# Optimization experiments

Hardware: AMD Instinct MI355X
Metric: run time of the kernel (lower is better)

## Reference

```python
import jax, jax.numpy as jnp
import numpy as np

B, N, C_IN, C_OUT, K, D_EMB = 64, 2048, 64, 64, 3, 10

def setup_inputs() -> dict:
    key = jax.random.key(0)
    k1, k2, k3, k4 = jax.random.split(key, 4)
    x = jax.random.normal(k1, (B, N, C_IN), dtype=jnp.float32)
    node_embeddings = jax.random.normal(k2, (N, D_EMB), dtype=jnp.float32)
    weights_pool = jax.random.normal(k3, (D_EMB, K, C_IN, C_OUT), dtype=jnp.float32) * 0.1
    bias_pool = jax.random.normal(k4, (D_EMB, C_OUT), dtype=jnp.float32) * 0.1
    return {"x": x, "node_embeddings": node_embeddings,
            "weights_pool": weights_pool, "bias_pool": bias_pool, "cheb_k": K}

def reference(x, node_embeddings, weights_pool, bias_pool, cheb_k):
    n = node_embeddings.shape[0]
    # adaptive adjacency: softmax over rows of relu(E E^T)
    supports = jax.nn.softmax(jax.nn.relu(node_embeddings @ node_embeddings.T), axis=1)  # [N,N]
    support_set = [jnp.eye(n, dtype=x.dtype), supports]
    for _ in range(2, cheb_k):
        support_set.append(2.0 * supports @ support_set[-1] - support_set[-2])
    supports_k = jnp.stack(support_set, axis=0)                     # [K,N,N]
    # per-node weights/bias generated from embedding
    weights = jnp.einsum('nd,dkio->nkio', node_embeddings, weights_pool)  # [N,K,Ci,Co]
    bias = node_embeddings @ bias_pool                               # [N,Co]
    # graph conv: gather Chebyshev-filtered features then per-node grouped GEMM
    x_g = jnp.einsum('knm,bmc->bnkc', supports_k, x)                 # [B,N,K,Ci]
    out = jnp.einsum('bnki,nkio->bno', x_g, weights) + bias          # [B,N,Co]
    return out
```

## Files before the change

### kernel.cpp

```cpp
#include <hip/hip_runtime.h>

typedef __attribute__((ext_vector_type(8))) short short8;
typedef __attribute__((ext_vector_type(4))) float f32x4;
typedef __attribute__((ext_vector_type(4))) unsigned short us4;
typedef __attribute__((ext_vector_type(8))) unsigned short us8;

constexpr int Bb = 64, Nn = 2048, CI = 64, CO = 64, KK = 3, DE = 10;
constexpr int NW = Bb * CI;
constexpr int WPSZ = KK * CI * CO;

__device__ __forceinline__ unsigned short f2bf(float f) {
  unsigned u = __float_as_uint(f);
  u += 0x7fff + ((u >> 16) & 1);
  return (unsigned short)(u >> 16);
}
__device__ __forceinline__ float bf2f(unsigned short h) {
  return __uint_as_float(((unsigned)h) << 16);
}
__device__ __forceinline__ void gl2lds16(const void* g, void* l) {
  __builtin_amdgcn_global_load_lds(
      (const __attribute__((address_space(1))) void*)g,
      (__attribute__((address_space(3))) void*)l, 16, 0, 0);
}

__global__ __launch_bounds__(256) void prep_kernel(
    const float* __restrict__ E, unsigned short* __restrict__ S,
    const float* __restrict__ x, unsigned short* __restrict__ Xrow,
    unsigned short* __restrict__ XT, const float* __restrict__ Wp,
    unsigned short* __restrict__ Wpf) {
  __shared__ float sh[5376];
  const int bid = blockIdx.x, t = threadIdx.x;

  if (bid < 2048) {
    const int n = bid;
    float emb[DE];
#pragma unroll
    for (int d = 0; d < DE; d++) emb[d] = E[n * DE + d];

    float v[8];
    for (int h = 0; h < 4; h++) {
      __syncthreads();
      const float* src = E + (size_t)(512 * DE) * h;
#pragma unroll
      for (int q = 0; q < 5; q++) {
        const int idx = t + q * 256;
        *(float4*)&sh[idx * 4] = *(const float4*)(src + idx * 4);
      }
      __syncthreads();
#pragma unroll
      for (int jj = 0; jj < 2; jj++) {
        const int lm = t + jj * 256;
        const float2* er = (const float2*)&sh[lm * 10];
        float dot = 0.f;
#pragma unroll
        for (int p = 0; p < 5; p++) {
          const float2 e2 = er[p];
          dot += emb[2 * p] * e2.x + emb[2 * p + 1] * e2.y;
        }
        v[h * 2 + jj] = fmaxf(dot, 0.f);
      }
    }

    float* red = &sh[5120];
    float lmax = -1e30f;
#pragma unroll
    for (int j = 0; j < 8; j++) lmax = fmaxf(lmax, v[j]);
    red[t] = lmax;
    __syncthreads();
    for (int s = 128; s > 0; s >>= 1) {
      if (t < s) red[t] = fmaxf(red[t], red[t + s]);
      __syncthreads();
    }
    const float rowmax = red[0];
    __syncthreads();
    float lsum = 0.f;
#pragma unroll
    for (int j = 0; j < 8; j++) { v[j] = __expf(v[j] - rowmax); lsum += v[j]; }
    red[t] = lsum;
    __syncthreads();
    for (int s = 128; s > 0; s >>= 1) {
      if (t < s) red[t] += red[t + s];
      __syncthreads();
    }
    const float inv = 1.f / red[0];
#pragma unroll
    for (int j = 0; j < 8; j++) S[(size_t)n * Nn + t + j * 256] = f2bf(v[j] * inv);
  } else if (bid < 4096) {
    const int id = bid - 2048;
    const int b = id & 63, n0 = (id >> 6) * 64;
    const int i4 = (t & 15) * 4;
#pragma unroll
    for (int j = 0; j < 4; j++) {
      const int r = j * 16 + (t >> 4);
      const float4 v =
          *(const float4*)(x + (size_t)b * (Nn * CI) + (size_t)(n0 + r) * CI + i4);
      us4 o; o.x = f2bf(v.x); o.y = f2bf(v.y); o.z = f2bf(v.z); o.w = f2bf(v.w);
      *(us4*)(Xrow + (size_t)(n0 + r) * NW + b * CI + i4) = o;
      sh[r * 65 + i4 + 0] = v.x; sh[r * 65 + i4 + 1] = v.y;
      sh[r * 65 + i4 + 2] = v.z; sh[r * 65 + i4 + 3] = v.w;
    }
    __syncthreads();
    const int i = t >> 2, c0 = (t & 3) * 16;
    us8 p0, p1;
#pragma unroll
    for (int j = 0; j < 8; j++) p0[j] = f2bf(sh[(c0 + j) * 65 + i]);
#pragma unroll
    for (int j = 0; j < 8; j++) p1[j] = f2bf(sh[(c0 + 8 + j) * 65 + i]);
    unsigned short* dst = XT + (size_t)(b * CI + i) * Nn + n0 + c0;
    *(us8*)(dst) = p0;
    *(us8*)(dst + 8) = p1;
  } else {
    const int e4 = ((bid - 4096) * 256 + t) * 4;
    const int d = e4 / WPSZ;
    const int r = e4 - d * WPSZ;
    const int c = r >> 12, io = r & 4095;
    float4 v = *(const float4*)(Wp + (size_t)d * WPSZ + c * 4096 + io);
    if (c == 0) {
      const float4 w2 = *(const float4*)(Wp + (size_t)d * WPSZ + 2 * 4096 + io);
      v.x -= w2.x; v.y -= w2.y; v.z -= w2.z; v.w -= w2.w;
    } else if (c == 2) {
      v.x *= 2.f; v.y *= 2.f; v.z *= 2.f; v.w *= 2.f;
    }
    us4 o; o.x = f2bf(v.x); o.y = f2bf(v.y); o.z = f2bf(v.z); o.w = f2bf(v.w);
    *(us4*)(Wpf + e4) = o;
  }
}

__global__ __launch_bounds__(256) void mfma_gemm(
    const unsigned short* __restrict__ A, const unsigned short* __restrict__ Bt,
    unsigned short* __restrict__ Crow, unsigned short* __restrict__ Ct, int mode) {
  __shared__ unsigned short sm[12288];
  unsigned short* As = sm;
  unsigned short* Bs = sm + 8192;
  const int t = threadIdx.x, lane = t & 63, wave = t >> 6;
  const int n0 = blockIdx.x * 64, m0 = blockIdx.y * 128;
  const int wm = (wave & 1) * 64, wn = (wave >> 1) * 32;
  const int lr = lane & 15, lq = lane >> 4;

  f32x4 acc[4][2] = {};
  const int srow = lane >> 3;
  const int schunk = (lane & 7) ^ srow;

  for (int k0 = 0; k0 < 2048; k0 += 64) {
    __syncthreads();
#pragma unroll
    for (int j = 0; j < 4; j++) {
      const int r0 = (wave * 4 + j) * 8;
      gl2lds16(A + (size_t)(m0 + r0 + srow) * 2048 + k0 + schunk * 8, As + r0 * 64);
    }
#pragma unroll
    for (int j = 0; j < 2; j++) {
      const int r0 = (wave * 2 + j) * 8;
      gl2lds16(Bt + (size_t)(n0 + r0 + srow) * 2048 + k0 + schunk * 8, Bs + r0 * 64);
    }
    __syncthreads();
#pragma unroll
    for (int ks = 0; ks < 2; ks++) {
      short8 af[4], bfr[2];
#pragma unroll
      for (int i = 0; i < 4; i++) {
        const int m = wm + i * 16 + lr;
        const int slot = (ks * 4 + lq) ^ (m & 7);
        af[i] = *(const short8*)(As + m * 64 + slot * 8);
      }
#pragma unroll
      for (int j = 0; j < 2; j++) {
        const int n = wn + j * 16 + lr;
        const int slot = (ks * 4 + lq) ^ (n & 7);
        bfr[j] = *(const short8*)(Bs + n * 64 + slot * 8);
      }
#pragma unroll
      for (int i = 0; i < 4; i++)
#pragma unroll
        for (int j = 0; j < 2; j++)
          acc[i][j] = __builtin_amdgcn_mfma_f32_16x16x32_bf16(af[i], bfr[j], acc[i][j], 0, 0, 0);
    }
  }

  __syncthreads();
#pragma unroll
  for (int i = 0; i < 4; i++) {
#pragma unroll
    for (int r = 0; r < 4; r++) {
      const int m = wm + i * 16 + lq * 4 + r;
      const int sw = (m & 7) ^ ((m >> 3) & 7);
#pragma unroll
      for (int j = 0; j < 2; j++) {
        const int n = wn + j * 16 + lr;
        sm[m * 64 + (((n >> 3) ^ sw) * 8) + (n & 7)] = f2bf(acc[i][j][r]);
      }
    }
  }
  __syncthreads();

  {
    const int rr = t >> 3, cc = (t & 7) * 8;
#pragma unroll
    for (int p = 0; p < 4; p++) {
      const int m = p * 32 + rr;
      const int slot = (cc >> 3) ^ (m & 7) ^ ((m >> 3) & 7);
      const us8 v = *(const us8*)(sm + m * 64 + slot * 8);
      *(us8*)(Crow + (size_t)(m0 + m) * NW + n0 + cc) = v;
    }
  }
  if (mode == 0) {
    const int mc = (t & 15) * 8;
#pragma unroll
    for (int p = 0; p < 4; p++) {
      const int n = p * 16 + (t >> 4);
      us8 v;
#pragma unroll
      for (int q = 0; q < 8; q++) {
        const int m = mc + q;
        v[q] = sm[m * 64 + (((n >> 3) ^ (m & 7) ^ ((m >> 3) & 7)) * 8) + (n & 7)];
      }
      *(us8*)(Ct + (size_t)(n0 + n) * 2048 + m0 + mc) = v;
    }
  }
}

__global__ __launch_bounds__(256) void out_kernel(
    const unsigned short* __restrict__ Xrow, const unsigned short* __restrict__ XG1,
    const unsigned short* __restrict__ Yr, const float* __restrict__ E,
    const unsigned short* __restrict__ Wpf, const float* __restrict__ bp,
    float* __restrict__ out) {
  __shared__ unsigned short Wt[KK * CO * 64];
  __shared__ unsigned short Al[KK * Bb * CI];
  __shared__ float biasl[CO];

  const int n = blockIdx.x, t = threadIdx.x, lane = t & 63, wave = t >> 6;

  const unsigned short* srcs[KK] = {Xrow + (size_t)n * NW, XG1 + (size_t)n * NW,
                                    Yr + (size_t)n * NW};
  const int srow = lane >> 3;
  const int schunk = (lane & 7) ^ srow;
#pragma unroll
  for (int j = 0; j < 6; j++) {
    const int r0 = (wave * 6 + j) * 8;
    const int c = r0 >> 6, b0 = r0 & 63;
    gl2lds16(srcs[c] + (b0 + srow) * 64 + schunk * 8, Al + r0 * 64);
  }

  float emb[DE];
#pragma unroll
  for (int d = 0; d < DE; d++) emb[d] = E[n * DE + d];

  const int o8 = (t & 7) * 8;
#pragma unroll
  for (int j = 0; j < 6; j++) {
    const int c = j >> 1;
    const int i = (j & 1) * 32 + (t >> 3);
    float w[8] = {};
#pragma unroll
    for (int d = 0; d < DE; d++) {
      const us8 wp = *(const us8*)(Wpf + (size_t)d * WPSZ + c * 4096 + i * 64 + o8);
#pragma unroll
      for (int q = 0; q < 8; q++) w[q] += emb[d] * bf2f(wp[q]);
    }
    const int chunk = i >> 3, ilo = i & 7;
#pragma unroll
    for (int q = 0; q < 8; q++) {
      const int o = o8 + q;
      Wt[(c * 64 + o) * 64 + ((chunk ^ (o & 7)) * 8) + ilo] = f2bf(w[q]);
    }
  }
  if (t < CO) {
    float bsum = 0.f;
#pragma unroll
    for (int d = 0; d < DE; d++) bsum += emb[d] * bp[d * CO + t];
    biasl[t] = bsum;
  }
  __syncthreads();

  const int lr = lane & 15, lq = lane >> 4;
  const float bias_o = biasl[wave * 16 + lr];
  f32x4 acc[4] = {};
#pragma unroll
  for (int kt = 0; kt < 6; kt++) {
    const int c = kt >> 1;
    const int chunk = (kt & 1) * 4 + lq;
    const int o = wave * 16 + lr;
    const short8 bfrag =
        *(const short8*)(Wt + (c * 64 + o) * 64 + (chunk ^ (o & 7)) * 8);
#pragma unroll
    for (int mt = 0; mt < 4; mt++) {
      const int b = mt * 16 + lr;
      const short8 afrag =
          *(const short8*)(Al + (c * 64 + b) * 64 + (chunk ^ (b & 7)) * 8);
      acc[mt] = __builtin_amdgcn_mfma_f32_16x16x32_bf16(afrag, bfrag, acc[mt], 0, 0, 0);
    }
  }

#pragma unroll
  for (int mt = 0; mt < 4; mt++) {
#pragma unroll
    for (int r = 0; r < 4; r++) {
      const int b = mt * 16 + lq * 4 + r;
      out[(size_t)b * (Nn * CO) + (size_t)n * CO + wave * 16 + lr] =
          acc[mt][r] + bias_o;
    }
  }
}

extern "C" void kernel_launch(void* const* d_in, const int* in_sizes, int n_in,
                              void* d_out, int out_size, void* d_ws,
                              size_t ws_size, hipStream_t stream) {
  const float* x  = (const float*)d_in[0];
  const float* E  = (const float*)d_in[1];
  const float* Wp = (const float*)d_in[2];
  const float* bp = (const float*)d_in[3];
  float* out = (float*)d_out;

  unsigned short* ws   = (unsigned short*)d_ws;
  unsigned short* Xrow = ws;
  unsigned short* XG1r = Xrow + (size_t)Nn * NW;
  unsigned short* Yr   = XG1r + (size_t)Nn * NW;
  unsigned short* S    = Yr   + (size_t)Nn * NW;
  unsigned short* XT   = S    + (size_t)Nn * Nn;
  unsigned short* XG1T = XT   + (size_t)NW * Nn;
  unsigned short* Wpf  = XG1T + (size_t)NW * Nn;

  prep_kernel<<<4216, 256, 0, stream>>>(E, S, x, Xrow, XT, Wp, Wpf);

  dim3 g(NW / 64, Nn / 128);
  mfma_gemm<<<g, 256, 0, stream>>>(S, XT,   XG1r, XG1T, 0);
  mfma_gemm<<<g, 256, 0, stream>>>(S, XG1T, Yr,   nullptr, 1);

  out_kernel<<<Nn, 256, 0, stream>>>(Xrow, XG1r, Yr, E, Wpf, bp, out);
}
```

Measured before the change: 215.0 us.

## Use wave-shuffle softmax reductions, swap GEMM grid order, stage output through LDS

The softmax row reductions in the prep kernel now use wave-level xor shuffles plus a four-entry shared combine. This replaces the tree reductions, which needed many block barriers. The GEMM grid swaps its x and y axes so consecutive blocks walk along the M dimension and share the same B column tile, which may change L2 reuse. The output kernel stages its accumulators in LDS, then writes float4 vectors with the bias added, so stores are coalesced and not scattered scalars. This adds two barriers and some LDS traffic in exchange.

```diff
diff --git a/kernel.cpp b/kernel.cpp
--- a/kernel.cpp
+++ b/kernel.cpp
@@ -33,6 +33,7 @@
 
   if (bid < 2048) {
     const int n = bid;
+    const int lane = t & 63, wv = t >> 6;
     float emb[DE];
 #pragma unroll
     for (int d = 0; d < DE; d++) emb[d] = E[n * DE + d];
@@ -61,28 +62,23 @@
       }
     }
 
-    float* red = &sh[5120];
-    float lmax = -1e30f;
-#pragma unroll
-    for (int j = 0; j < 8; j++) lmax = fmaxf(lmax, v[j]);
-    red[t] = lmax;
-    __syncthreads();
-    for (int s = 128; s > 0; s >>= 1) {
-      if (t < s) red[t] = fmaxf(red[t], red[t + s]);
-      __syncthreads();
-    }
-    const float rowmax = red[0];
-    __syncthreads();
+    float r = -1e30f;
+#pragma unroll
+    for (int j = 0; j < 8; j++) r = fmaxf(r, v[j]);
+#pragma unroll
+    for (int off = 32; off; off >>= 1) r = fmaxf(r, __shfl_xor(r, off));
+    if (lane == 0) sh[5120 + wv] = r;
+    __syncthreads();
+    const float rowmax = fmaxf(fmaxf(sh[5120], sh[5121]), fmaxf(sh[5122], sh[5123]));
+
     float lsum = 0.f;
 #pragma unroll
     for (int j = 0; j < 8; j++) { v[j] = __expf(v[j] - rowmax); lsum += v[j]; }
-    red[t] = lsum;
-    __syncthreads();
-    for (int s = 128; s > 0; s >>= 1) {
-      if (t < s) red[t] += red[t + s];
-      __syncthreads();
-    }
-    const float inv = 1.f / red[0];
+#pragma unroll
+    for (int off = 32; off; off >>= 1) lsum += __shfl_xor(lsum, off);
+    if (lane == 0) sh[5128 + wv] = lsum;
+    __syncthreads();
+    const float inv = 1.f / (sh[5128] + sh[5129] + sh[5130] + sh[5131]);
 #pragma unroll
     for (int j = 0; j < 8; j++) S[(size_t)n * Nn + t + j * 256] = f2bf(v[j] * inv);
   } else if (bid < 4096) {
@@ -133,7 +129,7 @@
   unsigned short* As = sm;
   unsigned short* Bs = sm + 8192;
   const int t = threadIdx.x, lane = t & 63, wave = t >> 6;
-  const int n0 = blockIdx.x * 64, m0 = blockIdx.y * 128;
+  const int m0 = blockIdx.x * 128, n0 = blockIdx.y * 64;
   const int wm = (wave & 1) * 64, wn = (wave >> 1) * 32;
   const int lr = lane & 15, lq = lane >> 4;
 
@@ -273,7 +269,6 @@
   __syncthreads();
 
   const int lr = lane & 15, lq = lane >> 4;
-  const float bias_o = biasl[wave * 16 + lr];
   f32x4 acc[4] = {};
 #pragma unroll
   for (int kt = 0; kt < 6; kt++) {
@@ -291,14 +286,23 @@
     }
   }
 
+  __syncthreads();
+  float* F = (float*)Wt;
+#pragma unroll
+  for (int mt = 0; mt < 4; mt++)
+#pragma unroll
+    for (int r = 0; r < 4; r++)
+      F[(mt * 16 + lq * 4 + r) * 68 + wave * 16 + lr] = acc[mt][r];
+  __syncthreads();
+
+  const int bo = t >> 4, o4 = (t & 15) * 4;
 #pragma unroll
   for (int mt = 0; mt < 4; mt++) {
-#pragma unroll
-    for (int r = 0; r < 4; r++) {
-      const int b = mt * 16 + lq * 4 + r;
-      out[(size_t)b * (Nn * CO) + (size_t)n * CO + wave * 16 + lr] =
-          acc[mt][r] + bias_o;
-    }
+    const int b = mt * 16 + bo;
+    float4 v = *(const float4*)&F[b * 68 + o4];
+    v.x += biasl[o4 + 0]; v.y += biasl[o4 + 1];
+    v.z += biasl[o4 + 2]; v.w += biasl[o4 + 3];
+    *(float4*)(out + (size_t)b * (Nn * CO) + (size_t)n * CO + o4) = v;
   }
 }
 
@@ -322,7 +326,7 @@
 
   prep_kernel<<<4216, 256, 0, stream>>>(E, S, x, Xrow, XT, Wp, Wpf);
 
-  dim3 g(NW / 64, Nn / 128);
+  dim3 g(Nn / 128, NW / 64);
   mfma_gemm<<<g, 256, 0, stream>>>(S, XT,   XG1r, XG1T, 0);
   mfma_gemm<<<g, 256, 0, stream>>>(S, XG1T, Yr,   nullptr, 1);
 
```

Measured after the change: 223.6 us. 4.0% more time.
